# Kernel tuning notes

Measured on AMD Instinct MI355X. Metric: run time of the kernel, lower is better.

Reference implementation:

```python
import jax, jax.numpy as jnp
import numpy as np

B, S, D_IN = 2, 2048, 1024
HIDDEN, H, HKV = 1024, 16, 4
R = H // HKV          # query heads per kv head
HD = HIDDEN // H      # head_dim = 64
D_OUT = 1024
SCALE = HD ** -0.5


def setup_inputs() -> dict:
    key = jax.random.key(0)
    ks = jax.random.split(key, 5)
    x = jax.random.normal(ks[0], (B, S, D_IN), dtype=jnp.float32)
    # store weights as (in, out); torch Linear computes x @ W.T with W (out,in)
    Wq = jax.random.normal(ks[1], (D_IN, HIDDEN), dtype=jnp.float32) * 0.02
    Wk = jax.random.normal(ks[2], (D_IN, HKV * HD), dtype=jnp.float32) * 0.02
    Wv = jax.random.normal(ks[3], (D_IN, HKV * HD), dtype=jnp.float32) * 0.02
    Wo = jax.random.normal(ks[4], (HIDDEN, D_OUT), dtype=jnp.float32) * 0.02
    return {"x": x, "Wq": Wq, "Wk": Wk, "Wv": Wv, "Wo": Wo}


def reference(x, Wq, Wk, Wv, Wo):
    # projections
    q = x @ Wq                                   # (B,S,H*HD)
    k = x @ Wk                                   # (B,S,HKV*HD)
    v = x @ Wv
    # repeat_interleave maps query head h -> kv head h // R,
    # so split query heads as (HKV, R) groups and broadcast KV.
    q = q.reshape(B, S, HKV, R, HD)
    k = k.reshape(B, S, HKV, HD)
    v = v.reshape(B, S, HKV, HD)
    attn = jnp.einsum('bskrd,btkd->bkrst', q, k) * SCALE   # (B,HKV,R,S,S)
    attn = jax.nn.softmax(attn, axis=-1)
    o = jnp.einsum('bkrst,btkd->bskrd', attn, v)           # (B,S,HKV,R,HD)
    o = o.reshape(B, S, HIDDEN)
    return o @ Wo                                          # (B,S,D_OUT)
```

## Files before the change

kernel.cpp:

```cpp
#include <hip/hip_runtime.h>

using u16 = unsigned short;
using u32 = unsigned int;
typedef __bf16 bf16x8 __attribute__((ext_vector_type(8)));
typedef u16 u16x8 __attribute__((ext_vector_type(8)));
typedef u32 u32x2 __attribute__((ext_vector_type(2)));
typedef u32 u32x4 __attribute__((ext_vector_type(4)));
typedef float f32x4 __attribute__((ext_vector_type(4)));
typedef float f32x16 __attribute__((ext_vector_type(16)));

#define B_   2
#define S_   2048
#define DIN  1024
#define HID  1024
#define NH   16
#define NKV  4
#define HD_  64
#define QKVW 1536
#define QSCL 0.1803368801111244f

__device__ __forceinline__ u16 f2b(float f) {
  u32 u = __builtin_bit_cast(u32, f);
  u32 r = (u + 0x7FFFu + ((u >> 16) & 1u)) >> 16;
  return (u16)r;
}

__device__ __forceinline__ void gl16(const void* g, void* l) {
  __builtin_amdgcn_global_load_lds(
      (const __attribute__((address_space(1))) void*)g,
      (__attribute__((address_space(3))) void*)l, 16, 0, 0);
}

__global__ void k_cvt(const float* __restrict__ in, u16* __restrict__ out, int n8) {
  int i = blockIdx.x * 256 + threadIdx.x;
  if (i >= n8) return;
  const float4* p = (const float4*)(in + (size_t)i * 8);
  float4 a = p[0], b = p[1];
  u16x8 o;
  o[0] = f2b(a.x); o[1] = f2b(a.y); o[2] = f2b(a.z); o[3] = f2b(a.w);
  o[4] = f2b(b.x); o[5] = f2b(b.y); o[6] = f2b(b.z); o[7] = f2b(b.w);
  *(u16x8*)(out + (size_t)i * 8) = o;
}

__global__ __launch_bounds__(256) void k_cvt_t3(
    const float* __restrict__ Wq, const float* __restrict__ Wk,
    const float* __restrict__ Wv, u16* __restrict__ WT)
{
  __shared__ float t[32][33];
  const int k0 = blockIdx.x * 32, n0 = blockIdx.y * 32;
  const float* W; int N, nb;
  if (n0 < HID)             { W = Wq; N = HID; nb = n0; }
  else if (n0 < HID + 256)  { W = Wk; N = 256; nb = n0 - HID; }
  else                      { W = Wv; N = 256; nb = n0 - HID - 256; }
  const int c = threadIdx.x & 31, r8 = threadIdx.x >> 5;
#pragma unroll
  for (int i = 0; i < 4; ++i)
    t[r8 + i * 8][c] = W[(size_t)(k0 + r8 + i * 8) * N + nb + c];
  __syncthreads();
#pragma unroll
  for (int i = 0; i < 4; ++i)
    WT[(size_t)(n0 + r8 + i * 8) * DIN + k0 + c] = f2b(t[c][r8 + i * 8]);
}

__global__ __launch_bounds__(256) void k_cvt_t(const float* __restrict__ W, u16* __restrict__ WT, int K, int N) {
  __shared__ float t[32][33];
  const int k0 = blockIdx.x * 32, n0 = blockIdx.y * 32;
  const int c = threadIdx.x & 31, r8 = threadIdx.x >> 5;
#pragma unroll
  for (int i = 0; i < 4; ++i)
    t[r8 + i * 8][c] = W[(size_t)(k0 + r8 + i * 8) * N + n0 + c];
  __syncthreads();
#pragma unroll
  for (int i = 0; i < 4; ++i)
    WT[(size_t)(n0 + r8 + i * 8) * K + k0 + c] = f2b(t[c][r8 + i * 8]);
}

__global__ __launch_bounds__(256) void k_vt(const u16* __restrict__ QKV, u16* __restrict__ Vt) {
  __shared__ u16 t[32][33];
  const int s0 = blockIdx.x * 32;
  const int d0 = blockIdx.y * 32;
  const int z  = blockIdx.z;
  const int b = z >> 2, kv = z & 3;
  const int c = threadIdx.x & 31, r8 = threadIdx.x >> 5;
#pragma unroll
  for (int i = 0; i < 4; ++i)
    t[r8 + i * 8][c] = QKV[(size_t)(b * S_ + s0 + r8 + i * 8) * QKVW + (HID + NKV * HD_) + kv * HD_ + d0 + c];
  __syncthreads();
#pragma unroll
  for (int i = 0; i < 4; ++i)
    Vt[(size_t)(z * HD_ + d0 + r8 + i * 8) * S_ + s0 + c] = t[c][r8 + i * 8];
}

template <typename OutT>
__global__ __launch_bounds__(256, 4) void k_gemm_bt(
    const u16* __restrict__ A, const u16* __restrict__ Bt,
    OutT* __restrict__ C, int M, int N, int K, int scaleCols, float scl)
{
  __shared__ u16 lA[2][128 * 32];
  __shared__ u16 lB[2][64 * 32];
  const int tid  = threadIdx.x;
  const int lane = tid & 63;
  const int wave = tid >> 6;
  const int wm = wave >> 1, wn = wave & 1;
  const int g = lane >> 4, li = lane & 15;
  const int bm = blockIdx.y * 128, bn = blockIdx.x * 64;
  const int arow = wave * 16 + (lane >> 2);
  const int acol = (lane & 3) * 8;

  f32x4 acc[4][2];
#pragma unroll
  for (int i = 0; i < 4; ++i)
#pragma unroll
    for (int j = 0; j < 2; ++j) acc[i][j] = f32x4{0.f, 0.f, 0.f, 0.f};

  const u16* Ab = A + (size_t)bm * K;
  const u16* Bb = Bt + (size_t)bn * K;

  auto stage = [&](int k0, int buf) {
#pragma unroll
    for (int h = 0; h < 2; ++h)
      gl16(&Ab[(size_t)(h * 64 + arow) * K + k0 + acol], (char*)lA[buf] + h * 4096 + wave * 1024);
    gl16(&Bb[(size_t)arow * K + k0 + acol], (char*)lB[buf] + wave * 1024);
  };

  stage(0, 0);
  __syncthreads();

  int cur = 0;
  for (int k0 = 0; k0 < K; k0 += 32) {
    if (k0 + 32 < K) stage(k0 + 32, cur ^ 1);
    bf16x8 af[4], bfr[2];
#pragma unroll
    for (int mt = 0; mt < 4; ++mt)
      af[mt] = *(const bf16x8*)&lA[cur][(wm * 64 + mt * 16 + li) * 32 + g * 8];
#pragma unroll
    for (int nt = 0; nt < 2; ++nt)
      bfr[nt] = *(const bf16x8*)&lB[cur][(wn * 32 + nt * 16 + li) * 32 + g * 8];
    __builtin_amdgcn_s_setprio(1);
#pragma unroll
    for (int mt = 0; mt < 4; ++mt)
#pragma unroll
      for (int nt = 0; nt < 2; ++nt)
        acc[mt][nt] = __builtin_amdgcn_mfma_f32_16x16x32_bf16(af[mt], bfr[nt], acc[mt][nt], 0, 0, 0);
    __builtin_amdgcn_s_setprio(0);
    __syncthreads();
    cur ^= 1;
  }

#pragma unroll
  for (int mt = 0; mt < 4; ++mt)
#pragma unroll
    for (int nt = 0; nt < 2; ++nt)
#pragma unroll
      for (int r = 0; r < 4; ++r) {
        int row = bm + wm * 64 + mt * 16 + g * 4 + r;
        int col = bn + wn * 32 + nt * 16 + li;
        float v = acc[mt][nt][r];
        if (col < scaleCols) v *= scl;
        if constexpr (sizeof(OutT) == 4) C[(size_t)row * N + col] = v;
        else                             C[(size_t)row * N + col] = f2b(v);
      }
}

__global__ __launch_bounds__(256, 2) void k_attn(
    const u16* __restrict__ QKV, const u16* __restrict__ Vt_g, u16* __restrict__ O)
{
  __shared__ u16 K_lds[3][64 * 64];
  __shared__ u16 Vt_lds[3][64 * 64];
  const int tid  = threadIdx.x;
  const int lane = tid & 63;
  const int w    = tid >> 6;
  const int lq = lane & 31;
  const int hi = lane >> 5;
  const int swl = (lq & 7) << 3;
  const int hx = (hi * 8) ^ (swl & 8);
  const int s0 = blockIdx.x * 32;
  const int kv = blockIdx.y;
  const int b  = blockIdx.z;
  const int hq = kv * 4 + w;

  int dcol[4];
#pragma unroll
  for (int d0 = 0; d0 < 4; ++d0) dcol[d0] = (d0 * 16) ^ (swl & 48);

  bf16x8 qf[4];
  {
    const u16* qb = QKV + (size_t)(b * S_ + s0 + lq) * QKVW + hq * HD_ + hi * 8;
#pragma unroll
    for (int d0 = 0; d0 < 4; ++d0) qf[d0] = *(const bf16x8*)(qb + d0 * 16);
  }

  float l = 0.f;
  f32x16 oacc0 = {}, oacc1 = {};
  bf16x8 pa[4];

  const int sr8 = lane >> 3;
  const int scol = ((lane & 7) ^ sr8) * 8;
  const int srow = w * 16;
  const u16* kge = QKV + (size_t)(b * S_) * QKVW + HID + kv * HD_;
  const u16* vge = Vt_g + (size_t)((b * NKV + kv) * HD_) * S_;

  auto stage = [&](int t, int buf) {
#pragma unroll
    for (int h = 0; h < 2; ++h) {
      gl16(kge + (size_t)(t * 64 + srow + h * 8 + sr8) * QKVW + scol,
           (char*)K_lds[buf] + srow * 128 + h * 1024);
      gl16(vge + (size_t)(srow + h * 8 + sr8) * S_ + t * 64 + scol,
           (char*)Vt_lds[buf] + srow * 128 + h * 1024);
    }
  };

  stage(0, 0);
  __syncthreads();

#define PK(dst, x, y) asm("v_cvt_pk_bf16_f32 %0, %1, %2" : "=v"(dst) : "v"(x), "v"(y))
  constexpr int NT = S_ / 64;
  int cb = 0;
  for (int t = 0; t < NT; ++t) {
    int nb = cb + 1; if (nb == 3) nb = 0;
    int pb = cb - 1; if (pb < 0) pb = 2;
    if (t + 1 < NT) stage(t + 1, nb);

    f32x16 st0 = {}, st1 = {};
    const u16* Kc = K_lds[cb];
    __builtin_amdgcn_s_setprio(1);
#pragma unroll
    for (int d0 = 0; d0 < 4; ++d0) {
      bf16x8 kf0 = *(const bf16x8*)&Kc[lq * 64 + dcol[d0] + hx];
      bf16x8 kf1 = *(const bf16x8*)&Kc[(32 + lq) * 64 + dcol[d0] + hx];
      st0 = __builtin_amdgcn_mfma_f32_32x32x16_bf16(kf0, qf[d0], st0, 0, 0, 0);
      st1 = __builtin_amdgcn_mfma_f32_32x32x16_bf16(kf1, qf[d0], st1, 0, 0, 0);
    }

#pragma unroll
    for (int i = 0; i < 16; ++i) st0[i] = __builtin_amdgcn_exp2f(st0[i]);
#pragma unroll
    for (int i = 0; i < 16; ++i) st1[i] = __builtin_amdgcn_exp2f(st1[i]);
    float s8[8];
#pragma unroll
    for (int i = 0; i < 8; ++i)
      s8[i] = (st0[i] + st0[i + 8]) + (st1[i] + st1[i + 8]);
    s8[0] += s8[4]; s8[1] += s8[5]; s8[2] += s8[6]; s8[3] += s8[7];
    l += (s8[0] + s8[1]) + (s8[2] + s8[3]);

    if (t > 0) {
      const u16* Vc = Vt_lds[pb];
#pragma unroll
      for (int ks = 0; ks < 4; ++ks) {
        bf16x8 vf0 = *(const bf16x8*)&Vc[lq * 64 + dcol[ks] + hx];
        bf16x8 vf1 = *(const bf16x8*)&Vc[(32 + lq) * 64 + dcol[ks] + hx];
        oacc0 = __builtin_amdgcn_mfma_f32_32x32x16_bf16(pa[ks], vf0, oacc0, 0, 0, 0);
        oacc1 = __builtin_amdgcn_mfma_f32_32x32x16_bf16(pa[ks], vf1, oacc1, 0, 0, 0);
      }
    }
    __builtin_amdgcn_s_setprio(0);

#pragma unroll
    for (int kb2 = 0; kb2 < 2; ++kb2) {
      const f32x16& ev = kb2 ? st1 : st0;
      u32 a0, a1, b0, b1;
      u32x2 r0, r1;
      u32x4 wv;
      PK(a0, ev[0], ev[1]);  PK(a1, ev[2], ev[3]);
      PK(b0, ev[4], ev[5]);  PK(b1, ev[6], ev[7]);
      r0 = __builtin_amdgcn_permlane32_swap(a0, b0, false, false);
      r1 = __builtin_amdgcn_permlane32_swap(a1, b1, false, false);
      wv[0] = r0[0]; wv[1] = r1[0]; wv[2] = r0[1]; wv[3] = r1[1];
      pa[kb2 * 2] = __builtin_bit_cast(bf16x8, wv);
      PK(a0, ev[8],  ev[9]);  PK(a1, ev[10], ev[11]);
      PK(b0, ev[12], ev[13]); PK(b1, ev[14], ev[15]);
      r0 = __builtin_amdgcn_permlane32_swap(a0, b0, false, false);
      r1 = __builtin_amdgcn_permlane32_swap(a1, b1, false, false);
      wv[0] = r0[0]; wv[1] = r1[0]; wv[2] = r0[1]; wv[3] = r1[1];
      pa[kb2 * 2 + 1] = __builtin_bit_cast(bf16x8, wv);
    }

    __syncthreads();
    cb = nb;
  }
#undef PK

  {
    int pb = cb - 1; if (pb < 0) pb = 2;
    const u16* Vc = Vt_lds[pb];
    __builtin_amdgcn_s_setprio(1);
#pragma unroll
    for (int ks = 0; ks < 4; ++ks) {
      bf16x8 vf0 = *(const bf16x8*)&Vc[lq * 64 + dcol[ks] + hx];
      bf16x8 vf1 = *(const bf16x8*)&Vc[(32 + lq) * 64 + dcol[ks] + hx];
      oacc0 = __builtin_amdgcn_mfma_f32_32x32x16_bf16(pa[ks], vf0, oacc0, 0, 0, 0);
      oacc1 = __builtin_amdgcn_mfma_f32_32x32x16_bf16(pa[ks], vf1, oacc1, 0, 0, 0);
    }
    __builtin_amdgcn_s_setprio(0);
  }

  l += __shfl_xor(l, 32);
  const size_t obase = (size_t)(b * S_ + s0) * HID + hq * HD_ + lq;
#pragma unroll
  for (int r = 0; r < 16; ++r) {
    const int qrow = (r & 3) + 8 * (r >> 2) + 4 * hi;
    float lr = __shfl(l, qrow);
    float inv = __builtin_amdgcn_rcpf(lr);
    O[obase + (size_t)qrow * HID]      = f2b(oacc0[r] * inv);
    O[obase + (size_t)qrow * HID + 32] = f2b(oacc1[r] * inv);
  }
}

extern "C" void kernel_launch(void* const* d_in, const int* in_sizes, int n_in,
                              void* d_out, int out_size, void* d_ws, size_t ws_size,
                              hipStream_t stream) {
  (void)in_sizes; (void)n_in; (void)out_size; (void)ws_size;
  const float* x  = (const float*)d_in[0];
  const float* Wq = (const float*)d_in[1];
  const float* Wk = (const float*)d_in[2];
  const float* Wv = (const float*)d_in[3];
  const float* Wo = (const float*)d_in[4];
  float* out = (float*)d_out;

  const size_t M = (size_t)B_ * S_;
  u16* xb    = (u16*)d_ws;
  u16* WqkvT = xb    + M * DIN;
  u16* WoT   = WqkvT + (size_t)QKVW * DIN;
  u16* QKV   = WoT   + (size_t)HID * HID;
  u16* Ob    = QKV   + M * QKVW;
  u16* Vt    = Ob    + M * HID;

  k_cvt<<<dim3((int)(M * DIN / 8 / 256)), 256, 0, stream>>>(x, xb, (int)(M * DIN / 8));
  k_cvt_t3<<<dim3(DIN / 32, QKVW / 32), 256, 0, stream>>>(Wq, Wk, Wv, WqkvT);
  k_cvt_t<<<dim3(HID / 32, HID / 32),   256, 0, stream>>>(Wo, WoT, HID, HID);

  k_gemm_bt<u16><<<dim3(QKVW / 64, (int)(M / 128)), 256, 0, stream>>>(
      xb, WqkvT, QKV, (int)M, QKVW, DIN, HID, QSCL);

  k_vt<<<dim3(S_ / 32, HD_ / 32, B_ * NKV), 256, 0, stream>>>(QKV, Vt);

  k_attn<<<dim3(S_ / 32, NKV, B_), 256, 0, stream>>>(QKV, Vt, Ob);

  k_gemm_bt<float><<<dim3(HID / 64, (int)(M / 128)), 256, 0, stream>>>(
      Ob, WoT, out, (int)M, HID, HID, 0, 1.0f);
}
```

Baseline: 107.4 us.

## Rework projection GEMM to 32x32 MFMA with swizzled LDS and merge weight converts

Result: slower. 118.8 us (+10.7%).

```diff
diff --git a/kernel.cpp b/kernel.cpp
--- a/kernel.cpp
+++ b/kernel.cpp
@@ -42,16 +42,18 @@
   *(u16x8*)(out + (size_t)i * 8) = o;
 }
 
-__global__ __launch_bounds__(256) void k_cvt_t3(
+__global__ __launch_bounds__(256) void k_cvt_tw(
     const float* __restrict__ Wq, const float* __restrict__ Wk,
-    const float* __restrict__ Wv, u16* __restrict__ WT)
+    const float* __restrict__ Wv, const float* __restrict__ Wo,
+    u16* __restrict__ WqkvT, u16* __restrict__ WoT)
 {
   __shared__ float t[32][33];
   const int k0 = blockIdx.x * 32, n0 = blockIdx.y * 32;
-  const float* W; int N, nb;
-  if (n0 < HID)             { W = Wq; N = HID; nb = n0; }
-  else if (n0 < HID + 256)  { W = Wk; N = 256; nb = n0 - HID; }
-  else                      { W = Wv; N = 256; nb = n0 - HID - 256; }
+  const float* W; int N, nb, drow; u16* dst;
+  if (n0 < HID)            { W = Wq; N = HID; nb = n0;              dst = WqkvT; drow = n0; }
+  else if (n0 < HID + 256) { W = Wk; N = 256; nb = n0 - HID;        dst = WqkvT; drow = n0; }
+  else if (n0 < QKVW)      { W = Wv; N = 256; nb = n0 - HID - 256;  dst = WqkvT; drow = n0; }
+  else                     { W = Wo; N = HID; nb = n0 - QKVW;       dst = WoT;   drow = n0 - QKVW; }
   const int c = threadIdx.x & 31, r8 = threadIdx.x >> 5;
 #pragma unroll
   for (int i = 0; i < 4; ++i)
@@ -59,20 +61,7 @@
   __syncthreads();
 #pragma unroll
   for (int i = 0; i < 4; ++i)
-    WT[(size_t)(n0 + r8 + i * 8) * DIN + k0 + c] = f2b(t[c][r8 + i * 8]);
-}
-
-__global__ __launch_bounds__(256) void k_cvt_t(const float* __restrict__ W, u16* __restrict__ WT, int K, int N) {
-  __shared__ float t[32][33];
-  const int k0 = blockIdx.x * 32, n0 = blockIdx.y * 32;
-  const int c = threadIdx.x & 31, r8 = threadIdx.x >> 5;
-#pragma unroll
-  for (int i = 0; i < 4; ++i)
-    t[r8 + i * 8][c] = W[(size_t)(k0 + r8 + i * 8) * N + n0 + c];
-  __syncthreads();
-#pragma unroll
-  for (int i = 0; i < 4; ++i)
-    WT[(size_t)(n0 + r8 + i * 8) * K + k0 + c] = f2b(t[c][r8 + i * 8]);
+    dst[(size_t)(drow + r8 + i * 8) * DIN + k0 + c] = f2b(t[c][r8 + i * 8]);
 }
 
 __global__ __launch_bounds__(256) void k_vt(const u16* __restrict__ QKV, u16* __restrict__ Vt) {
@@ -92,35 +81,37 @@
 }
 
 template <typename OutT>
-__global__ __launch_bounds__(256, 4) void k_gemm_bt(
+__global__ __launch_bounds__(128, 3) void k_gemm_bt(
     const u16* __restrict__ A, const u16* __restrict__ Bt,
     OutT* __restrict__ C, int M, int N, int K, int scaleCols, float scl)
 {
-  __shared__ u16 lA[2][128 * 32];
-  __shared__ u16 lB[2][64 * 32];
+  __shared__ u16 lA[2][64 * 32];
+  __shared__ u16 lB[2][128 * 32];
   const int tid  = threadIdx.x;
   const int lane = tid & 63;
-  const int wave = tid >> 6;
-  const int wm = wave >> 1, wn = wave & 1;
-  const int g = lane >> 4, li = lane & 15;
-  const int bm = blockIdx.y * 128, bn = blockIdx.x * 64;
-  const int arow = wave * 16 + (lane >> 2);
-  const int acol = (lane & 3) * 8;
-
-  f32x4 acc[4][2];
-#pragma unroll
-  for (int i = 0; i < 4; ++i)
-#pragma unroll
-    for (int j = 0; j < 2; ++j) acc[i][j] = f32x4{0.f, 0.f, 0.f, 0.f};
+  const int w    = tid >> 6;
+  const int rl = lane & 31, hi = lane >> 5;
+  const int bm = blockIdx.y * 64, bn = blockIdx.x * 128;
+
+  f32x16 acc[2][2] = {};
 
   const u16* Ab = A + (size_t)bm * K;
   const u16* Bb = Bt + (size_t)bn * K;
 
+  const int srow_l = lane >> 2;
+  const int schunk = ((lane & 3) ^ ((lane >> 2) & 3)) * 8;
+
   auto stage = [&](int k0, int buf) {
 #pragma unroll
-    for (int h = 0; h < 2; ++h)
-      gl16(&Ab[(size_t)(h * 64 + arow) * K + k0 + acol], (char*)lA[buf] + h * 4096 + wave * 1024);
-    gl16(&Bb[(size_t)arow * K + k0 + acol], (char*)lB[buf] + wave * 1024);
+    for (int h = 0; h < 2; ++h) {
+      const int sl = h * 2 + w;
+      gl16(&Ab[(size_t)(sl * 16 + srow_l) * K + k0 + schunk], (char*)lA[buf] + sl * 1024);
+    }
+#pragma unroll
+    for (int h = 0; h < 4; ++h) {
+      const int sl = h * 2 + w;
+      gl16(&Bb[(size_t)(sl * 16 + srow_l) * K + k0 + schunk], (char*)lB[buf] + sl * 1024);
+    }
   };
 
   stage(0, 0);
@@ -129,33 +120,39 @@
   int cur = 0;
   for (int k0 = 0; k0 < K; k0 += 32) {
     if (k0 + 32 < K) stage(k0 + 32, cur ^ 1);
-    bf16x8 af[4], bfr[2];
-#pragma unroll
-    for (int mt = 0; mt < 4; ++mt)
-      af[mt] = *(const bf16x8*)&lA[cur][(wm * 64 + mt * 16 + li) * 32 + g * 8];
-#pragma unroll
-    for (int nt = 0; nt < 2; ++nt)
-      bfr[nt] = *(const bf16x8*)&lB[cur][(wn * 32 + nt * 16 + li) * 32 + g * 8];
+    bf16x8 af[2][2], bfr[2][2];
+#pragma unroll
+    for (int kk = 0; kk < 2; ++kk) {
+      const int cc = ((kk * 2 + hi) ^ (rl & 3)) * 8;
+#pragma unroll
+      for (int m = 0; m < 2; ++m)
+        af[m][kk] = *(const bf16x8*)&lA[cur][(m * 32 + rl) * 32 + cc];
+#pragma unroll
+      for (int n = 0; n < 2; ++n)
+        bfr[n][kk] = *(const bf16x8*)&lB[cur][(w * 64 + n * 32 + rl) * 32 + cc];
+    }
     __builtin_amdgcn_s_setprio(1);
 #pragma unroll
-    for (int mt = 0; mt < 4; ++mt)
-#pragma unroll
-      for (int nt = 0; nt < 2; ++nt)
-        acc[mt][nt] = __builtin_amdgcn_mfma_f32_16x16x32_bf16(af[mt], bfr[nt], acc[mt][nt], 0, 0, 0);
+    for (int kk = 0; kk < 2; ++kk)
+#pragma unroll
+      for (int m = 0; m < 2; ++m)
+#pragma unroll
+        for (int n = 0; n < 2; ++n)
+          acc[m][n] = __builtin_amdgcn_mfma_f32_32x32x16_bf16(af[m][kk], bfr[n][kk], acc[m][n], 0, 0, 0);
     __builtin_amdgcn_s_setprio(0);
     __syncthreads();
     cur ^= 1;
   }
 
 #pragma unroll
-  for (int mt = 0; mt < 4; ++mt)
-#pragma unroll
-    for (int nt = 0; nt < 2; ++nt)
-#pragma unroll
-      for (int r = 0; r < 4; ++r) {
-        int row = bm + wm * 64 + mt * 16 + g * 4 + r;
-        int col = bn + wn * 32 + nt * 16 + li;
-        float v = acc[mt][nt][r];
+  for (int m = 0; m < 2; ++m)
+#pragma unroll
+    for (int n = 0; n < 2; ++n)
+#pragma unroll
+      for (int r = 0; r < 16; ++r) {
+        int row = bm + m * 32 + (r & 3) + 8 * (r >> 2) + 4 * hi;
+        int col = bn + w * 64 + n * 32 + rl;
+        float v = acc[m][n][r];
         if (col < scaleCols) v *= scl;
         if constexpr (sizeof(OutT) == 4) C[(size_t)row * N + col] = v;
         else                             C[(size_t)row * N + col] = f2b(v);
@@ -326,16 +323,15 @@
   u16* Vt    = Ob    + M * HID;
 
   k_cvt<<<dim3((int)(M * DIN / 8 / 256)), 256, 0, stream>>>(x, xb, (int)(M * DIN / 8));
-  k_cvt_t3<<<dim3(DIN / 32, QKVW / 32), 256, 0, stream>>>(Wq, Wk, Wv, WqkvT);
-  k_cvt_t<<<dim3(HID / 32, HID / 32),   256, 0, stream>>>(Wo, WoT, HID, HID);
-
-  k_gemm_bt<u16><<<dim3(QKVW / 64, (int)(M / 128)), 256, 0, stream>>>(
+  k_cvt_tw<<<dim3(DIN / 32, (QKVW + HID) / 32), 256, 0, stream>>>(Wq, Wk, Wv, Wo, WqkvT, WoT);
+
+  k_gemm_bt<u16><<<dim3(QKVW / 128, (int)(M / 64)), 128, 0, stream>>>(
       xb, WqkvT, QKV, (int)M, QKVW, DIN, HID, QSCL);
 
   k_vt<<<dim3(S_ / 32, HD_ / 32, B_ * NKV), 256, 0, stream>>>(QKV, Vt);
 
   k_attn<<<dim3(S_ / 32, NKV, B_), 256, 0, stream>>>(QKV, Vt, Ob);
 
-  k_gemm_bt<float><<<dim3(HID / 64, (int)(M / 128)), 256, 0, stream>>>(
+  k_gemm_bt<float><<<dim3(HID / 128, (int)(M / 64)), 128, 0, stream>>>(
       Ob, WoT, out, (int)M, HID, HID, 0, 1.0f);
 }
```
